# Kernel optimization log

Measured on AMD Instinct MI355X. Metric: run time of the kernel, lower is better.

Reference implementation:

```python
import math
import jax, jax.numpy as jnp
import numpy as np

B, S = 4, 2048
D_MODEL, D_STATE = 1024, 256
KSIZE, CHUNK, STEPS = 5, 16, 2
TOPK, LOOKBACK = 8, 64


def setup_inputs() -> dict:
    key = jax.random.key(0)
    ks = jax.random.split(key, 12)
    gn = lambda k, shape, s: jax.random.normal(k, shape, jnp.float32) * s
    s_in = 1.0 / math.sqrt(D_MODEL)
    s_st = 1.0 / math.sqrt(D_STATE)
    inp = {}
    inp['x'] = gn(ks[0], (B, S, D_MODEL), 1.0)
    inp['Wi'] = gn(ks[1], (D_MODEL, D_STATE), s_in); inp['bi'] = jnp.zeros((D_STATE,), jnp.float32)
    inp['conv_w'] = gn(ks[2], (KSIZE, D_STATE), 1.0 / math.sqrt(KSIZE)); inp['conv_b'] = jnp.zeros((D_STATE,), jnp.float32)
    inp['Wp'] = gn(ks[3], (D_STATE, D_STATE), s_st); inp['bp'] = jnp.zeros((D_STATE,), jnp.float32)
    inp['Wh'] = gn(ks[4], (D_STATE, 3), s_st); inp['bh'] = jnp.zeros((3,), jnp.float32)
    inp['Wq'] = gn(ks[5], (D_STATE, D_STATE), s_st); inp['bq'] = jnp.zeros((D_STATE,), jnp.float32)
    inp['Wk'] = gn(ks[6], (D_STATE, D_STATE), s_st); inp['bk'] = jnp.zeros((D_STATE,), jnp.float32)
    inp['Wv'] = gn(ks[7], (D_STATE, D_STATE), s_st); inp['bv'] = jnp.zeros((D_STATE,), jnp.float32)
    inp['W1'] = gn(ks[8], (4 * D_STATE, D_STATE), 1.0 / math.sqrt(4 * D_STATE)); inp['b1'] = jnp.zeros((D_STATE,), jnp.float32)
    inp['W2'] = gn(ks[9], (D_STATE, D_STATE), s_st); inp['b2'] = jnp.zeros((D_STATE,), jnp.float32)
    # original zero-inits out_proj; use small random so outputs/grads are nontrivial
    inp['Wo'] = gn(ks[10], (D_STATE, D_MODEL), 0.02 * s_st); inp['bo'] = jnp.zeros((D_MODEL,), jnp.float32)
    return inp


def _forward(x, Wi, bi, conv_w, conv_b, Wp, bp, Wh, bh, Wq, bq, Wk, bk, Wv, bv, W1, b1, W2, b2, Wo, bo):
    bsz, seq, _ = x.shape
    dim = Wi.shape[1]
    h = x @ Wi + bi  # [B,S,Dstate]
    # banded window indices: window for token t covers tokens [t-LOOKBACK, t)
    pos = jnp.arange(seq)[:, None] + jnp.arange(LOOKBACK)[None, :]  # index into LOOKBACK-left-padded seq
    valid = (pos - LOOKBACK) >= 0  # [S,L] actual token index = pos - LOOKBACK, always < t
    cidx = jnp.arange(seq)[:, None] + jnp.arange(KSIZE)[None, :]
    scale = 1.0 / math.sqrt(dim)
    for _ in range(STEPS):
        # causal depthwise conv (left pad K-1)
        hp = jnp.pad(h, ((0, 0), (KSIZE - 1, 0), (0, 0)))
        mixed = jnp.einsum('bskd,kd->bsd', hp[:, cidx, :], conv_w) + conv_b
        # phrase pool: chunk means, project, broadcast back to tokens
        ph = h.reshape(bsz, seq // CHUNK, CHUNK, dim).mean(axis=2)
        pb = jnp.repeat(ph @ Wp + bp, CHUNK, axis=1)
        # semantic causal windowed top-k attention
        q = h @ Wq + bq
        k = h @ Wk + bk
        v = h @ Wv + bv
        kp = jnp.pad(k, ((0, 0), (LOOKBACK, 0), (0, 0)))
        scores = jnp.einsum('bsd,bsld->bsl', q, kp[:, pos, :]) * scale  # [B,S,L]
        scores = jnp.where(valid[None], scores, -jnp.inf)
        ts, tr = jax.lax.top_k(scores, TOPK)  # [B,S,K]
        m = ts.max(axis=-1, keepdims=True)
        e = jnp.exp(ts - jnp.where(jnp.isfinite(m), m, 0.0))  # -inf slots -> 0 weight
        w = e / jnp.maximum(e.sum(axis=-1, keepdims=True), 1e-30)  # token 0: all zero
        tok = jnp.clip(jnp.arange(seq)[None, :, None] - LOOKBACK + tr, 0, seq - 1)  # [B,S,K]
        vg = jnp.take_along_axis(v, tok.reshape(bsz, seq * TOPK, 1), axis=1).reshape(bsz, seq, TOPK, dim)
        summ = jnp.einsum('bsk,bskd->bsd', w, vg)
        # update MLP with halt gate
        ui = jnp.concatenate([h, mixed, pb, summ], axis=-1)
        delta = jnp.tanh(ui @ W1 + b1) @ W2 + b2
        gate = jax.nn.sigmoid(h @ Wh + bh)[..., 2:3]  # halt_gate channel
        h = h + delta * gate
    return x + (h @ Wo + bo)


def reference(x, Wi, bi, conv_w, conv_b, Wp, bp, Wh, bh, Wq, bq, Wk, bk, Wv, bv, W1, b1, W2, b2, Wo, bo):
    return _forward(x, Wi, bi, conv_w, conv_b, Wp, bp, Wh, bh, Wq, bq, Wk, bk, Wv, bv, W1, b1, W2, b2, Wo, bo)
```

## Files before the change

### kernel.cpp

```cpp
#include <hip/hip_runtime.h>
#include <math.h>

#define B_    4
#define S_    2048
#define BS_   8192
#define DM_   1024
#define DS_   256
#define LB_   64
#define TOPK_ 8

typedef unsigned short u16;
typedef __bf16 bf16x8 __attribute__((ext_vector_type(8)));
typedef float  f32x4  __attribute__((ext_vector_type(4)));

static __device__ __forceinline__ u16 f2bf(float f) {
    union { float f; unsigned u; } a; a.f = f;
    unsigned u = a.u;
    unsigned r = u + 0x7FFFu + ((u >> 16) & 1u);
    return (u16)(r >> 16);
}
static __device__ __forceinline__ float bf2f(u16 v) {
    union { unsigned u; float f; } a; a.u = ((unsigned)v) << 16; return a.f;
}
static __device__ __forceinline__ unsigned pack2(float a, float b) {
    return (unsigned)f2bf(a) | ((unsigned)f2bf(b) << 16);
}

#define GLD16(g, l) __builtin_amdgcn_global_load_lds(                         \
    (const __attribute__((address_space(1))) void*)(g),                       \
    (__attribute__((address_space(3))) void*)(l), 16, 0, 0)

template<int MF, int EPI>
__device__ __forceinline__ void epilogue(
    f32x4 (&acc)[MF][2], int bm, int bn, int wm, int wn, int lr, int lc,
    const float* __restrict__ bias, void* __restrict__ Cv, int N,
    const void* __restrict__ extra0v, const float* __restrict__ extra1)
{
    #pragma unroll
    for (int i = 0; i < MF; ++i) {
        #pragma unroll
        for (int j = 0; j < 2; ++j) {
            int col = bn + wn * 32 + j * 16 + lr;
            #pragma unroll
            for (int r = 0; r < 4; ++r) {
                int row = bm + wm * (MF * 16) + i * 16 + lc * 4 + r;
                float val = acc[i][j][r] + bias[col];
                if constexpr (EPI == 2) {
                    const u16* e0 = (const u16*)extra0v;
                    val = bf2f(e0[(size_t)row * N + col]) + val * extra1[row];
                    ((u16*)Cv)[(size_t)row * N + col] = f2bf(val);
                } else if constexpr (EPI == 3) {
                    const u16* e0 = (const u16*)extra0v;
                    ((float*)Cv)[(size_t)row * N + col] = bf2f(e0[(size_t)row * N + col]) + val;
                } else {
                    ((u16*)Cv)[(size_t)row * N + col] = f2bf(val);
                }
            }
        }
    }
}

__device__ __forceinline__ void slab_mfma(
    unsigned char* smA, unsigned char* smB, f32x4 (&acc)[2][2],
    int wm, int wn, int lr, int lc)
{
    #pragma unroll
    for (int kg = 0; kg < 8; ++kg) {
        bf16x8 af[2], bfr[2];
        #pragma unroll
        for (int i = 0; i < 2; ++i) {
            int m = wm * 32 + i * 16 + lr;
            af[i] = *reinterpret_cast<const bf16x8*>(
                smA + m * 512 + (((kg * 4 + lc) ^ (m & 15)) * 16));
        }
        #pragma unroll
        for (int j = 0; j < 2; ++j) {
            int n = wn * 32 + j * 16 + lr;
            bfr[j] = *reinterpret_cast<const bf16x8*>(
                smB + n * 512 + (((kg * 4 + lc) ^ (n & 15)) * 16));
        }
        #pragma unroll
        for (int i = 0; i < 2; ++i)
            #pragma unroll
            for (int j = 0; j < 2; ++j)
                acc[i][j] = __builtin_amdgcn_mfma_f32_16x16x32_bf16(
                    af[i], bfr[j], acc[i][j], 0, 0, 0);
    }
}

template<int EPI>
__device__ __forceinline__ void mm256_dev(
    unsigned char* smem, int id, int nb, int gx,
    const u16* __restrict__ A, const u16* __restrict__ Bt,
    const float* __restrict__ bias, void* __restrict__ Cv,
    int N, const void* __restrict__ extra0v, const float* __restrict__ extra1)
{
    unsigned char* smA = smem;
    unsigned char* smB = smem + 32768;

    const int per = nb >> 3;
    const int nid = (id & 7) * per + (id >> 3);
    const int bx  = nid % gx, by = nid / gx;

    const int lane = threadIdx.x & 63, wid = threadIdx.x >> 6;
    const int wm   = wid >> 1, wn = wid & 1;
    const int bm   = by * 64, bn = bx * 64;
    const int lr   = lane & 15, lc = lane >> 4;
    const int lrow2 = lane >> 5;
    const int g_lin = lane & 31;

    #pragma unroll
    for (int t = 0; t < 8; ++t) {
        int rbase = wid * 16 + t * 2;
        int row   = rbase + lrow2;
        int gg    = g_lin ^ (row & 15);
        GLD16(A + (size_t)(bm + row) * 256 + gg * 8, smA + (size_t)rbase * 512);
    }
    #pragma unroll
    for (int t = 0; t < 8; ++t) {
        int rbase = wid * 16 + t * 2;
        int row   = rbase + lrow2;
        int gg    = g_lin ^ (row & 15);
        GLD16(Bt + (size_t)(bn + row) * 256 + gg * 8, smB + (size_t)rbase * 512);
    }
    __syncthreads();

    f32x4 acc[2][2] = {};
    slab_mfma(smA, smB, acc, wm, wn, lr, lc);

    epilogue<2, EPI>(acc, bm, bn, wm, wn, lr, lc, bias, Cv, N, extra0v, extra1);
}

template<int EPI>
__global__ __launch_bounds__(256) void mm256_k(
    const u16* __restrict__ A, const u16* __restrict__ Bt,
    const float* __restrict__ bias, void* __restrict__ Cv,
    int N, int gx,
    const void* __restrict__ extra0v, const float* __restrict__ extra1)
{
    __shared__ __align__(16) unsigned char smem[65536];
    mm256_dev<EPI>(smem, blockIdx.x, gridDim.x, gx, A, Bt, bias, Cv, N,
                   extra0v, extra1);
}

template<int EPI>
__global__ __launch_bounds__(256) void mm1024_k(
    const u16* __restrict__ A, const u16* __restrict__ Bt,
    const float* __restrict__ bias, void* __restrict__ Cv,
    int N, int gx,
    const void* __restrict__ extra0v, const float* __restrict__ extra1)
{
    __shared__ __align__(16) unsigned char smem[65536];
    unsigned char* smA = smem;
    unsigned char* smB = smem + 32768;

    const int nb  = gridDim.x;
    const int per = nb >> 3;
    const int id  = blockIdx.x;
    const int nid = (id & 7) * per + (id >> 3);
    const int bx  = nid % gx, by = nid / gx;

    const int lane = threadIdx.x & 63, wid = threadIdx.x >> 6;
    const int wm   = wid >> 1, wn = wid & 1;
    const int bm   = by * 64, bn = bx * 64;
    const int lr   = lane & 15, lc = lane >> 4;
    const int lrow2 = lane >> 5;
    const int g_lin = lane & 31;

    f32x4 acc[2][2] = {};

    #pragma unroll
    for (int s = 0; s < 4; ++s) {
        if (s) __syncthreads();
        #pragma unroll
        for (int t = 0; t < 8; ++t) {
            int rbase = wid * 16 + t * 2;
            int row   = rbase + lrow2;
            int gg    = g_lin ^ (row & 15);
            GLD16(A + (size_t)(bm + row) * 1024 + s * 256 + gg * 8,
                  smA + (size_t)rbase * 512);
        }
        #pragma unroll
        for (int t = 0; t < 8; ++t) {
            int rbase = wid * 16 + t * 2;
            int row   = rbase + lrow2;
            int gg    = g_lin ^ (row & 15);
            GLD16(Bt + (size_t)(bn + row) * 1024 + s * 256 + gg * 8,
                  smB + (size_t)rbase * 512);
        }
        __syncthreads();
        slab_mfma(smA, smB, acc, wm, wn, lr, lc);
    }

    epilogue<2, EPI>(acc, bm, bn, wm, wn, lr, lc, bias, Cv, N, extra0v, extra1);
}

__global__ __launch_bounds__(256) void mm_ui_k(
    const u16* __restrict__ h, const u16* __restrict__ mixed,
    const u16* __restrict__ php, const u16* __restrict__ summ,
    const u16* __restrict__ W1t, const float* __restrict__ b1,
    u16* __restrict__ t)
{
    __shared__ __align__(16) unsigned char smem[65536];
    unsigned char* smA = smem;
    unsigned char* smB = smem + 32768;

    const int nb  = gridDim.x;
    const int per = nb >> 3;
    const int id  = blockIdx.x;
    const int nid = (id & 7) * per + (id >> 3);
    const int bx  = nid & 3, by = nid >> 2;

    const int lane = threadIdx.x & 63, wid = threadIdx.x >> 6;
    const int wm   = wid >> 1, wn = wid & 1;
    const int bm   = by * 64, bn = bx * 64;
    const int lr   = lane & 15, lc = lane >> 4;
    const int lrow2 = lane >> 5;
    const int g_lin = lane & 31;

    f32x4 acc[2][2] = {};

    #pragma unroll
    for (int s = 0; s < 4; ++s) {
        const u16* Asrc = (s == 0) ? h : (s == 1) ? mixed : (s == 2) ? php : summ;
        if (s) __syncthreads();
        #pragma unroll
        for (int tt = 0; tt < 8; ++tt) {
            int rbase = wid * 16 + tt * 2;
            int row   = rbase + lrow2;
            int gg    = g_lin ^ (row & 15);
            int rs    = bm + row;
            if (s == 2) rs >>= 4;
            GLD16(Asrc + (size_t)rs * 256 + gg * 8, smA + (size_t)rbase * 512);
        }
        #pragma unroll
        for (int tt = 0; tt < 8; ++tt) {
            int rbase = wid * 16 + tt * 2;
            int row   = rbase + lrow2;
            int gg    = g_lin ^ (row & 15);
            GLD16(W1t + (size_t)(bn + row) * 1024 + s * 256 + gg * 8,
                  smB + (size_t)rbase * 512);
        }
        __syncthreads();
        slab_mfma(smA, smB, acc, wm, wn, lr, lc);
    }

    #pragma unroll
    for (int i = 0; i < 2; ++i) {
        #pragma unroll
        for (int j = 0; j < 2; ++j) {
            int col = bn + wn * 32 + j * 16 + lr;
            #pragma unroll
            for (int r = 0; r < 4; ++r) {
                int row = bm + wm * 32 + i * 16 + lc * 4 + r;
                t[(size_t)row * DS_ + col] = f2bf(tanhf(acc[i][j][r] + b1[col]));
            }
        }
    }
}

__device__ __forceinline__ void conv_dev(
    unsigned char* smem, int cid,
    const u16* __restrict__ h, const float* __restrict__ conv_w,
    const float* __restrict__ conv_b, const float* __restrict__ Wh,
    const float* __restrict__ bh, const u16* __restrict__ Wpt,
    const float* __restrict__ bp, u16* __restrict__ mixed,
    u16* __restrict__ php, float* __restrict__ gate)
{
    float* gpart = (float*)smem;
    float* cm    = (float*)(smem + 256);
    const int blk = (cid & 7) * 64 + (cid >> 3);
    const int d = threadIdx.x;
    const int b = blk >> 7;
    const int s0 = (blk & 127) * 16;
    const u16* hb = h + (size_t)b * S_ * DS_;
    u16* mb = mixed + (size_t)b * S_ * DS_;

    const float w0 = conv_w[0 * DS_ + d], w1 = conv_w[1 * DS_ + d],
                w2 = conv_w[2 * DS_ + d], w3 = conv_w[3 * DS_ + d],
                w4 = conv_w[4 * DS_ + d];
    const float cb = conv_b[d];
    const float whd = Wh[d * 3 + 2];

    float a0 = (s0 >= 4) ? bf2f(hb[(size_t)(s0 - 4) * DS_ + d]) : 0.f;
    float a1 = (s0 >= 3) ? bf2f(hb[(size_t)(s0 - 3) * DS_ + d]) : 0.f;
    float a2 = (s0 >= 2) ? bf2f(hb[(size_t)(s0 - 2) * DS_ + d]) : 0.f;
    float a3 = (s0 >= 1) ? bf2f(hb[(size_t)(s0 - 1) * DS_ + d]) : 0.f;

    float sum = 0.f;
    #pragma unroll
    for (int tt = 0; tt < 16; ++tt) {
        int s = s0 + tt;
        float cur = bf2f(hb[(size_t)s * DS_ + d]);
        mb[(size_t)s * DS_ + d] = f2bf(w0 * a0 + w1 * a1 + w2 * a2 + w3 * a3 + w4 * cur + cb);
        sum += cur;
        float g = cur * whd;
        #pragma unroll
        for (int off = 32; off; off >>= 1) g += __shfl_down(g, off);
        if ((d & 63) == 0) gpart[tt * 4 + (d >> 6)] = g;
        a0 = a1; a1 = a2; a2 = a3; a3 = cur;
    }
    cm[d] = sum * (1.f / 16.f);
    __syncthreads();
    if (d < 16) {
        float gg = gpart[d * 4 + 0] + gpart[d * 4 + 1] + gpart[d * 4 + 2] + gpart[d * 4 + 3];
        gate[(size_t)b * S_ + s0 + d] = 1.f / (1.f + expf(-(gg + bh[2])));
    }
    float accp = bp[d];
    const u16* wr = Wpt + (size_t)d * 256;
    #pragma unroll
    for (int k = 0; k < 256; k += 8) {
        bf16x8 w8 = *reinterpret_cast<const bf16x8*>(wr + k);
        accp += cm[k]     * (float)w8[0] + cm[k + 1] * (float)w8[1]
              + cm[k + 2] * (float)w8[2] + cm[k + 3] * (float)w8[3]
              + cm[k + 4] * (float)w8[4] + cm[k + 5] * (float)w8[5]
              + cm[k + 6] * (float)w8[6] + cm[k + 7] * (float)w8[7];
    }
    php[(size_t)blk * DS_ + d] = f2bf(accp);
}

__global__ __launch_bounds__(256) void step_a_k(
    const u16* __restrict__ h, const u16* __restrict__ Wqkvt,
    const float* __restrict__ bqkv, u16* __restrict__ qkv,
    const float* __restrict__ conv_w, const float* __restrict__ conv_b,
    const float* __restrict__ Wh, const float* __restrict__ bh,
    const u16* __restrict__ Wpt, const float* __restrict__ bp,
    u16* __restrict__ mixed, u16* __restrict__ php, float* __restrict__ gate)
{
    __shared__ __align__(16) unsigned char smem[65536];
    if (blockIdx.x < 512) {
        conv_dev(smem, blockIdx.x, h, conv_w, conv_b, Wh, bh,
                 Wpt, bp, mixed, php, gate);
    } else {
        mm256_dev<0>(smem, blockIdx.x - 512, 1536, 12, h, Wqkvt, bqkv, qkv,
                     768, nullptr, nullptr);
    }
}

__global__ __launch_bounds__(256) void scores_k(
    const u16* __restrict__ qkv, float* __restrict__ scores)
{
    __shared__ __align__(16) unsigned char smem[65536];
    unsigned char* smQ = smem;
    unsigned char* smK = smem + 16384;
    float* Sld = reinterpret_cast<float*>(smem);

    const int bid = blockIdx.x;
    const int blk = (bid & 7) * 32 + (bid >> 3);
    const int t0 = blk * 32;
    const int b  = t0 >> 11;
    const int s0 = t0 & (S_ - 1);
    const int tid = threadIdx.x;
    const int lane = tid & 63, wid = tid >> 6;
    const int lr = lane & 15, lc = lane >> 4;
    const int qt  = wid & 1;
    const int ktb = (wid >> 1) * 3;
    const int lrow2 = lane >> 5;
    const int g_lin = lane & 31;

    #pragma unroll
    for (int t = 0; t < 4; ++t) {
        int rbase = wid * 8 + t * 2;
        int row   = rbase + lrow2;
        int gg    = g_lin ^ (row & 15);
        GLD16(qkv + (size_t)(t0 + row) * 768 + gg * 8,
              smQ + (size_t)rbase * 512);
    }
    #pragma unroll
    for (int t = 0; t < 12; ++t) {
        int rbase = wid * 24 + t * 2;
        int row   = rbase + lrow2;
        int krow  = s0 - 64 + row; if (krow < 0) krow = 0;
        int gg    = g_lin ^ (row & 15);
        GLD16(qkv + ((size_t)(b * S_) + krow) * 768 + 256 + gg * 8,
              smK + (size_t)rbase * 512);
    }
    __syncthreads();

    f32x4 acc[3] = {};
    #pragma unroll
    for (int ks = 0; ks < 8; ++ks) {
        int m = qt * 16 + lr;
        bf16x8 af = *reinterpret_cast<const bf16x8*>(
            smQ + m * 512 + (((ks * 4 + lc) ^ (m & 15)) * 16));
        #pragma unroll
        for (int j = 0; j < 3; ++j) {
            int n = (ktb + j) * 16 + lr;
            bf16x8 bv = *reinterpret_cast<const bf16x8*>(
                smK + n * 512 + (((ks * 4 + lc) ^ (n & 15)) * 16));
            acc[j] = __builtin_amdgcn_mfma_f32_16x16x32_bf16(af, bv, acc[j], 0, 0, 0);
        }
    }
    __syncthreads();

    #pragma unroll
    for (int j = 0; j < 3; ++j) {
        int col = (ktb + j) * 16 + lr;
        #pragma unroll
        for (int r = 0; r < 4; ++r) {
            int row = qt * 16 + lc * 4 + r;
            Sld[row * 97 + col] = acc[j][r];
        }
    }
    __syncthreads();

    #pragma unroll
    for (int it = 0; it < 8; ++it) {
        int e = tid + it * 256;
        int i = e >> 6, l = e & 63;
        scores[(size_t)(t0 + i) * 64 + l] = Sld[i * 97 + i + l] * 0.0625f;
    }
}

__global__ __launch_bounds__(256) void select_k(
    const float* __restrict__ scores, const u16* __restrict__ qkv,
    u16* __restrict__ summ)
{
    const int bid = blockIdx.x;
    const int sb  = (bid & 7) * 256 + (bid >> 3);
    const int m   = sb * 4 + (threadIdx.x >> 6);
    const int b = m >> 11;
    const int s = m & (S_ - 1);
    const int lane = threadIdx.x & 63;

    float v = (s - LB_ + lane >= 0) ? scores[(size_t)m * 64 + lane] : -INFINITY;
    int idx = lane;

    #pragma unroll
    for (int k = 2; k <= 64; k <<= 1) {
        #pragma unroll
        for (int j = k >> 1; j > 0; j >>= 1) {
            float ov = __shfl_xor(v, j);
            int   oi = __shfl_xor(idx, j);
            bool mineFirst = (v > ov) || (v == ov && idx < oi);
            bool lowLane  = (lane & j) == 0;
            bool dirFirst = (lane & k) == 0;
            bool keep = (lowLane == dirFirst) ? mineFirst : !mineFirst;
            if (!keep) { v = ov; idx = oi; }
        }
    }

    float vals[TOPK_]; int idxs[TOPK_];
    #pragma unroll
    for (int t = 0; t < TOPK_; ++t) {
        vals[t] = __shfl(v, t);
        idxs[t] = __shfl(idx, t);
    }

    const float mref = (vals[0] == -INFINITY) ? 0.f : vals[0];
    float e[TOPK_], ssum = 0.f;
    #pragma unroll
    for (int t = 0; t < TOPK_; ++t) { e[t] = expf(vals[t] - mref); ssum += e[t]; }
    const float inv = 1.f / fmaxf(ssum, 1e-30f);

    float o0 = 0.f, o1 = 0.f, o2 = 0.f, o3 = 0.f;
    #pragma unroll
    for (int t = 0; t < TOPK_; ++t) {
        float wt = e[t] * inv;
        int tok = s - LB_ + idxs[t];
        tok = min(max(tok, 0), S_ - 1);
        ushort4 vv = *reinterpret_cast<const ushort4*>(
            qkv + ((size_t)(b * S_) + tok) * 768 + 512 + lane * 4);
        o0 += wt * bf2f(vv.x);
        o1 += wt * bf2f(vv.y);
        o2 += wt * bf2f(vv.z);
        o3 += wt * bf2f(vv.w);
    }
    ushort4 pk;
    pk.x = f2bf(o0); pk.y = f2bf(o1); pk.z = f2bf(o2); pk.w = f2bf(o3);
    *reinterpret_cast<ushort4*>(summ + (size_t)m * DS_ + lane * 4) = pk;
}

__global__ __launch_bounds__(256) void prep_all_k(
    const float* __restrict__ x,
    const float* __restrict__ Wi, const float* __restrict__ Wq,
    const float* __restrict__ Wk, const float* __restrict__ Wv,
    const float* __restrict__ Wp, const float* __restrict__ W1,
    const float* __restrict__ W2, const float* __restrict__ Wo,
    const float* __restrict__ bq, const float* __restrict__ bk,
    const float* __restrict__ bv,
    u16* __restrict__ xb,
    u16* __restrict__ Wit, u16* __restrict__ Wqkvt, u16* __restrict__ Wpt,
    u16* __restrict__ W1t, u16* __restrict__ W2t, u16* __restrict__ Wot,
    float* __restrict__ bqkv)
{
    const int bid0 = blockIdx.x;
    if (bid0 < 4096) {
        int i = (bid0 * 256 + threadIdx.x) * 8;
        float4 a = *reinterpret_cast<const float4*>(x + i);
        float4 b = *reinterpret_cast<const float4*>(x + i + 4);
        uint4 g;
        g.x = pack2(a.x, a.y); g.y = pack2(a.z, a.w);
        g.z = pack2(b.x, b.y); g.w = pack2(b.z, b.w);
        *reinterpret_cast<uint4*>(xb + i) = g;
        return;
    }
    const int bid = bid0 - 4096;
    if (bid >= 1088) {
        for (int i = threadIdx.x; i < 768; i += 256) {
            float v = (i < 256) ? bq[i] : (i < 512) ? bk[i - 256] : bv[i - 512];
            bqkv[i] = v;
        }
        return;
    }
    const float* in; u16* out; int K, N, t;
    if (bid < 256)      { in = Wi; out = Wit;             K = 1024; N = 256;  t = bid; }
    else if (bid < 320) { in = Wq; out = Wqkvt;           K = 256;  N = 256;  t = bid - 256; }
    else if (bid < 384) { in = Wk; out = Wqkvt + 256*256; K = 256;  N = 256;  t = bid - 320; }
    else if (bid < 448) { in = Wv; out = Wqkvt + 512*256; K = 256;  N = 256;  t = bid - 384; }
    else if (bid < 512) { in = Wp; out = Wpt;             K = 256;  N = 256;  t = bid - 448; }
    else if (bid < 768) { in = W1; out = W1t;             K = 1024; N = 256;  t = bid - 512; }
    else if (bid < 832) { in = W2; out = W2t;             K = 256;  N = 256;  t = bid - 768; }
    else                { in = Wo; out = Wot;             K = 256;  N = 1024; t = bid - 832; }
    const int tilesX = N >> 5;
    const int n0 = (t % tilesX) * 32, k0 = (t / tilesX) * 32;
    __shared__ float tl[32][33];
    const int cx = threadIdx.x & 31, cy = threadIdx.x >> 5;
    #pragma unroll
    for (int r = 0; r < 32; r += 8)
        tl[cy + r][cx] = in[(size_t)(k0 + cy + r) * N + n0 + cx];
    __syncthreads();
    #pragma unroll
    for (int r = 0; r < 32; r += 8)
        out[(size_t)(n0 + cy + r) * K + k0 + cx] = f2bf(tl[cx][cy + r]);
}

extern "C" void kernel_launch(void* const* d_in, const int* in_sizes, int n_in,
                              void* d_out, int out_size, void* d_ws, size_t ws_size,
                              hipStream_t stream)
{
    const float* x      = (const float*)d_in[0];
    const float* Wi     = (const float*)d_in[1];
    const float* bi     = (const float*)d_in[2];
    const float* conv_w = (const float*)d_in[3];
    const float* conv_b = (const float*)d_in[4];
    const float* Wp     = (const float*)d_in[5];
    const float* bp     = (const float*)d_in[6];
    const float* Wh     = (const float*)d_in[7];
    const float* bh     = (const float*)d_in[8];
    const float* Wq     = (const float*)d_in[9];
    const float* bq     = (const float*)d_in[10];
    const float* Wk     = (const float*)d_in[11];
    const float* bk     = (const float*)d_in[12];
    const float* Wv     = (const float*)d_in[13];
    const float* bv     = (const float*)d_in[14];
    const float* W1     = (const float*)d_in[15];
    const float* b1     = (const float*)d_in[16];
    const float* W2     = (const float*)d_in[17];
    const float* b2     = (const float*)d_in[18];
    const float* Wo     = (const float*)d_in[19];
    const float* bo     = (const float*)d_in[20];
    float* out = (float*)d_out;

    char* p = (char*)d_ws;
    auto alloc = [&](size_t bytes) { char* r = p; p += (bytes + 255) & ~(size_t)255; return r; };

    u16*  xb     = (u16*)alloc((size_t)BS_ * DM_ * 2);
    u16*  h      = (u16*)alloc((size_t)BS_ * DS_ * 2);
    u16*  mixed  = (u16*)alloc((size_t)BS_ * DS_ * 2);
    u16*  qkv    = (u16*)alloc((size_t)BS_ * 768 * 2);
    u16*  sm     = (u16*)alloc((size_t)BS_ * DS_ * 2);
    u16*  tb     = (u16*)alloc((size_t)BS_ * DS_ * 2);
    u16*  php    = (u16*)alloc((size_t)512 * DS_ * 2);
    float* gate  = (float*)alloc((size_t)BS_ * 4);
    float* scores= (float*)alloc((size_t)BS_ * 64 * 4);
    float* bqkv  = (float*)alloc(768 * 4);
    u16* Wit     = (u16*)alloc((size_t)256 * 1024 * 2);
    u16* Wqkvt   = (u16*)alloc((size_t)768 * 256 * 2);
    u16* Wpt     = (u16*)alloc((size_t)256 * 256 * 2);
    u16* W1t     = (u16*)alloc((size_t)256 * 1024 * 2);
    u16* W2t     = (u16*)alloc((size_t)256 * 256 * 2);
    u16* Wot     = (u16*)alloc((size_t)1024 * 256 * 2);

    dim3 blk(256);

    prep_all_k<<<5185, blk, 0, stream>>>(x, Wi, Wq, Wk, Wv, Wp, W1, W2, Wo,
                                         bq, bk, bv, xb,
                                         Wit, Wqkvt, Wpt, W1t, W2t, Wot, bqkv);

    mm1024_k<0><<<512, blk, 0, stream>>>(xb, Wit, bi, h, DS_, 4, nullptr, nullptr);

    for (int step = 0; step < 2; ++step) {
        step_a_k<<<2048, blk, 0, stream>>>(h, Wqkvt, bqkv, qkv,
                                           conv_w, conv_b, Wh, bh, Wpt, bp,
                                           mixed, php, gate);
        scores_k<<<256, blk, 0, stream>>>(qkv, scores);
        select_k<<<2048, blk, 0, stream>>>(scores, qkv, sm);
        mm_ui_k<<<512, blk, 0, stream>>>(h, mixed, php, sm, W1t, b1, tb);
        mm256_k<2><<<512, blk, 0, stream>>>(tb, W2t, b2, h, DS_, 4, h, gate);
    }

    mm256_k<3><<<2048, blk, 0, stream>>>(h, Wot, bo, out, DM_, 16, xb, nullptr);
}
```

Before: 140.9 us.

## Widen GEMM tiles to reuse staged A slabs across multiple B column blocks

Each GEMM block (input projection, QKV, W1, W2, output projection) now covers 128 or 256 output columns instead of 64. It stages the A slab once and restages only the B slab for each extra 64-column sub-tile, and the grids shrink to match. The aim is to cut redundant A loads and the number of blocks launched. The cost is fewer blocks and extra serialized barrier/load phases per block with no overlap of the B restaging. Separately, the scores kernel splits its K-loop across two accumulators to expose more independent MFMA chains.

```diff
diff --git a/kernel.cpp b/kernel.cpp
--- a/kernel.cpp
+++ b/kernel.cpp
@@ -30,20 +30,20 @@
     (const __attribute__((address_space(1))) void*)(g),                       \
     (__attribute__((address_space(3))) void*)(l), 16, 0, 0)
 
-template<int MF, int EPI>
+template<int EPI>
 __device__ __forceinline__ void epilogue(
-    f32x4 (&acc)[MF][2], int bm, int bn, int wm, int wn, int lr, int lc,
+    f32x4 (&acc)[2][2], int bm, int bn, int wm, int wn, int lr, int lc,
     const float* __restrict__ bias, void* __restrict__ Cv, int N,
     const void* __restrict__ extra0v, const float* __restrict__ extra1)
 {
     #pragma unroll
-    for (int i = 0; i < MF; ++i) {
+    for (int i = 0; i < 2; ++i) {
         #pragma unroll
         for (int j = 0; j < 2; ++j) {
             int col = bn + wn * 32 + j * 16 + lr;
             #pragma unroll
             for (int r = 0; r < 4; ++r) {
-                int row = bm + wm * (MF * 16) + i * 16 + lc * 4 + r;
+                int row = bm + wm * 32 + i * 16 + lc * 4 + r;
                 float val = acc[i][j][r] + bias[col];
                 if constexpr (EPI == 2) {
                     const u16* e0 = (const u16*)extra0v;
@@ -60,7 +60,7 @@
     }
 }
 
-__device__ __forceinline__ void slab_mfma(
+__device__ __forceinline__ void slab_mfma1(
     unsigned char* smA, unsigned char* smB, f32x4 (&acc)[2][2],
     int wm, int wn, int lr, int lc)
 {
@@ -88,8 +88,21 @@
     }
 }
 
-template<int EPI>
-__device__ __forceinline__ void mm256_dev(
+__device__ __forceinline__ void stage_slab(
+    unsigned char* sm, const u16* __restrict__ src, int pitch,
+    int wid, int lrow2, int g_lin)
+{
+    #pragma unroll
+    for (int t = 0; t < 8; ++t) {
+        int rbase = wid * 16 + t * 2;
+        int row   = rbase + lrow2;
+        int gg    = g_lin ^ (row & 15);
+        GLD16(src + (size_t)row * pitch + gg * 8, sm + (size_t)rbase * 512);
+    }
+}
+
+template<int H, int EPI>
+__device__ __forceinline__ void mm256r_dev(
     unsigned char* smem, int id, int nb, int gx,
     const u16* __restrict__ A, const u16* __restrict__ Bt,
     const float* __restrict__ bias, void* __restrict__ Cv,
@@ -104,47 +117,44 @@
 
     const int lane = threadIdx.x & 63, wid = threadIdx.x >> 6;
     const int wm   = wid >> 1, wn = wid & 1;
-    const int bm   = by * 64, bn = bx * 64;
+    const int bm   = by * 64, bn = bx * (64 * H);
     const int lr   = lane & 15, lc = lane >> 4;
     const int lrow2 = lane >> 5;
     const int g_lin = lane & 31;
 
-    #pragma unroll
-    for (int t = 0; t < 8; ++t) {
-        int rbase = wid * 16 + t * 2;
-        int row   = rbase + lrow2;
-        int gg    = g_lin ^ (row & 15);
-        GLD16(A + (size_t)(bm + row) * 256 + gg * 8, smA + (size_t)rbase * 512);
-    }
-    #pragma unroll
-    for (int t = 0; t < 8; ++t) {
-        int rbase = wid * 16 + t * 2;
-        int row   = rbase + lrow2;
-        int gg    = g_lin ^ (row & 15);
-        GLD16(Bt + (size_t)(bn + row) * 256 + gg * 8, smB + (size_t)rbase * 512);
-    }
+    stage_slab(smA, A + (size_t)bm * 256, 256, wid, lrow2, g_lin);
+    stage_slab(smB, Bt + (size_t)bn * 256, 256, wid, lrow2, g_lin);
     __syncthreads();
 
-    f32x4 acc[2][2] = {};
-    slab_mfma(smA, smB, acc, wm, wn, lr, lc);
-
-    epilogue<2, EPI>(acc, bm, bn, wm, wn, lr, lc, bias, Cv, N, extra0v, extra1);
-}
-
-template<int EPI>
-__global__ __launch_bounds__(256) void mm256_k(
+    #pragma unroll
+    for (int ht = 0; ht < H; ++ht) {
+        f32x4 acc[2][2] = {};
+        slab_mfma1(smA, smB, acc, wm, wn, lr, lc);
+        if (ht + 1 < H) {
+            __syncthreads();
+            stage_slab(smB, Bt + (size_t)(bn + (ht + 1) * 64) * 256, 256,
+                       wid, lrow2, g_lin);
+        }
+        epilogue<EPI>(acc, bm, bn + ht * 64, wm, wn, lr, lc, bias, Cv, N,
+                      extra0v, extra1);
+        if (ht + 1 < H) __syncthreads();
+    }
+}
+
+template<int H, int EPI>
+__global__ __launch_bounds__(256) void mm256r_k(
     const u16* __restrict__ A, const u16* __restrict__ Bt,
     const float* __restrict__ bias, void* __restrict__ Cv,
     int N, int gx,
     const void* __restrict__ extra0v, const float* __restrict__ extra1)
 {
     __shared__ __align__(16) unsigned char smem[65536];
-    mm256_dev<EPI>(smem, blockIdx.x, gridDim.x, gx, A, Bt, bias, Cv, N,
-                   extra0v, extra1);
+    mm256r_dev<H, EPI>(smem, blockIdx.x, gridDim.x, gx, A, Bt, bias, Cv, N,
+                       extra0v, extra1);
 }
 
 template<int EPI>
-__global__ __launch_bounds__(256) void mm1024_k(
+__global__ __launch_bounds__(256) void mm1024r_k(
     const u16* __restrict__ A, const u16* __restrict__ Bt,
     const float* __restrict__ bias, void* __restrict__ Cv,
     int N, int gx,
@@ -162,37 +172,29 @@
 
     const int lane = threadIdx.x & 63, wid = threadIdx.x >> 6;
     const int wm   = wid >> 1, wn = wid & 1;
-    const int bm   = by * 64, bn = bx * 64;
+    const int bm   = by * 64, bn = bx * 128;
     const int lr   = lane & 15, lc = lane >> 4;
     const int lrow2 = lane >> 5;
     const int g_lin = lane & 31;
 
-    f32x4 acc[2][2] = {};
+    f32x4 acc0[2][2] = {}, acc1[2][2] = {};
 
     #pragma unroll
     for (int s = 0; s < 4; ++s) {
         if (s) __syncthreads();
-        #pragma unroll
-        for (int t = 0; t < 8; ++t) {
-            int rbase = wid * 16 + t * 2;
-            int row   = rbase + lrow2;
-            int gg    = g_lin ^ (row & 15);
-            GLD16(A + (size_t)(bm + row) * 1024 + s * 256 + gg * 8,
-                  smA + (size_t)rbase * 512);
-        }
-        #pragma unroll
-        for (int t = 0; t < 8; ++t) {
-            int rbase = wid * 16 + t * 2;
-            int row   = rbase + lrow2;
-            int gg    = g_lin ^ (row & 15);
-            GLD16(Bt + (size_t)(bn + row) * 1024 + s * 256 + gg * 8,
-                  smB + (size_t)rbase * 512);
-        }
+        stage_slab(smA, A + (size_t)bm * 1024 + s * 256, 1024, wid, lrow2, g_lin);
+        stage_slab(smB, Bt + (size_t)bn * 1024 + s * 256, 1024, wid, lrow2, g_lin);
         __syncthreads();
-        slab_mfma(smA, smB, acc, wm, wn, lr, lc);
-    }
-
-    epilogue<2, EPI>(acc, bm, bn, wm, wn, lr, lc, bias, Cv, N, extra0v, extra1);
+        slab_mfma1(smA, smB, acc0, wm, wn, lr, lc);
+        __syncthreads();
+        stage_slab(smB, Bt + (size_t)(bn + 64) * 1024 + s * 256, 1024,
+                   wid, lrow2, g_lin);
+        __syncthreads();
+        slab_mfma1(smA, smB, acc1, wm, wn, lr, lc);
+    }
+
+    epilogue<EPI>(acc0, bm, bn,      wm, wn, lr, lc, bias, Cv, N, extra0v, extra1);
+    epilogue<EPI>(acc1, bm, bn + 64, wm, wn, lr, lc, bias, Cv, N, extra0v, extra1);
 }
 
 __global__ __launch_bounds__(256) void mm_ui_k(
@@ -209,16 +211,16 @@
     const int per = nb >> 3;
     const int id  = blockIdx.x;
     const int nid = (id & 7) * per + (id >> 3);
-    const int bx  = nid & 3, by = nid >> 2;
+    const int bx  = nid & 1, by = nid >> 1;
 
     const int lane = threadIdx.x & 63, wid = threadIdx.x >> 6;
     const int wm   = wid >> 1, wn = wid & 1;
-    const int bm   = by * 64, bn = bx * 64;
+    const int bm   = by * 64, bn = bx * 128;
     const int lr   = lane & 15, lc = lane >> 4;
     const int lrow2 = lane >> 5;
     const int g_lin = lane & 31;
 
-    f32x4 acc[2][2] = {};
+    f32x4 acc0[2][2] = {}, acc1[2][2] = {};
 
     #pragma unroll
     for (int s = 0; s < 4; ++s) {
@@ -233,27 +235,29 @@
             if (s == 2) rs >>= 4;
             GLD16(Asrc + (size_t)rs * 256 + gg * 8, smA + (size_t)rbase * 512);
         }
-        #pragma unroll
-        for (int tt = 0; tt < 8; ++tt) {
-            int rbase = wid * 16 + tt * 2;
-            int row   = rbase + lrow2;
-            int gg    = g_lin ^ (row & 15);
-            GLD16(W1t + (size_t)(bn + row) * 1024 + s * 256 + gg * 8,
-                  smB + (size_t)rbase * 512);
-        }
+        stage_slab(smB, W1t + (size_t)bn * 1024 + s * 256, 1024, wid, lrow2, g_lin);
         __syncthreads();
-        slab_mfma(smA, smB, acc, wm, wn, lr, lc);
-    }
-
-    #pragma unroll
-    for (int i = 0; i < 2; ++i) {
-        #pragma unroll
-        for (int j = 0; j < 2; ++j) {
-            int col = bn + wn * 32 + j * 16 + lr;
+        slab_mfma1(smA, smB, acc0, wm, wn, lr, lc);
+        __syncthreads();
+        stage_slab(smB, W1t + (size_t)(bn + 64) * 1024 + s * 256, 1024,
+                   wid, lrow2, g_lin);
+        __syncthreads();
+        slab_mfma1(smA, smB, acc1, wm, wn, lr, lc);
+    }
+
+    #pragma unroll
+    for (int half = 0; half < 2; ++half) {
+        f32x4 (&acc)[2][2] = half ? acc1 : acc0;
+        #pragma unroll
+        for (int i = 0; i < 2; ++i) {
             #pragma unroll
-            for (int r = 0; r < 4; ++r) {
-                int row = bm + wm * 32 + i * 16 + lc * 4 + r;
-                t[(size_t)row * DS_ + col] = f2bf(tanhf(acc[i][j][r] + b1[col]));
+            for (int j = 0; j < 2; ++j) {
+                int col = bn + half * 64 + wn * 32 + j * 16 + lr;
+                #pragma unroll
+                for (int r = 0; r < 4; ++r) {
+                    int row = bm + wm * 32 + i * 16 + lc * 4 + r;
+                    t[(size_t)row * DS_ + col] = f2bf(tanhf(acc[i][j][r] + b1[col]));
+                }
             }
         }
     }
@@ -328,12 +332,12 @@
     u16* __restrict__ mixed, u16* __restrict__ php, float* __restrict__ gate)
 {
     __shared__ __align__(16) unsigned char smem[65536];
-    if (blockIdx.x < 512) {
-        conv_dev(smem, blockIdx.x, h, conv_w, conv_b, Wh, bh,
+    if (blockIdx.x < 768) {
+        mm256r_dev<2, 0>(smem, blockIdx.x, 768, 6, h, Wqkvt, bqkv, qkv,
+                         768, nullptr, nullptr);
+    } else {
+        conv_dev(smem, blockIdx.x - 768, h, conv_w, conv_b, Wh, bh,
                  Wpt, bp, mixed, php, gate);
-    } else {
-        mm256_dev<0>(smem, blockIdx.x - 512, 1536, 12, h, Wqkvt, bqkv, qkv,
-                     768, nullptr, nullptr);
     }
 }
 
@@ -377,18 +381,23 @@
     }
     __syncthreads();
 
-    f32x4 acc[3] = {};
-    #pragma unroll
-    for (int ks = 0; ks < 8; ++ks) {
+    f32x4 acc[3] = {}, acc2[3] = {};
+    #pragma unroll
+    for (int ks = 0; ks < 8; ks += 2) {
         int m = qt * 16 + lr;
-        bf16x8 af = *reinterpret_cast<const bf16x8*>(
-            smQ + m * 512 + (((ks * 4 + lc) ^ (m & 15)) * 16));
+        bf16x8 af0 = *reinterpret_cast<const bf16x8*>(
+            smQ + m * 512 + ((((ks + 0) * 4 + lc) ^ (m & 15)) * 16));
+        bf16x8 af1 = *reinterpret_cast<const bf16x8*>(
+            smQ + m * 512 + ((((ks + 1) * 4 + lc) ^ (m & 15)) * 16));
         #pragma unroll
         for (int j = 0; j < 3; ++j) {
             int n = (ktb + j) * 16 + lr;
-            bf16x8 bv = *reinterpret_cast<const bf16x8*>(
-                smK + n * 512 + (((ks * 4 + lc) ^ (n & 15)) * 16));
-            acc[j] = __builtin_amdgcn_mfma_f32_16x16x32_bf16(af, bv, acc[j], 0, 0, 0);
+            bf16x8 bv0 = *reinterpret_cast<const bf16x8*>(
+                smK + n * 512 + ((((ks + 0) * 4 + lc) ^ (n & 15)) * 16));
+            bf16x8 bv1 = *reinterpret_cast<const bf16x8*>(
+                smK + n * 512 + ((((ks + 1) * 4 + lc) ^ (n & 15)) * 16));
+            acc[j]  = __builtin_amdgcn_mfma_f32_16x16x32_bf16(af0, bv0, acc[j], 0, 0, 0);
+            acc2[j] = __builtin_amdgcn_mfma_f32_16x16x32_bf16(af1, bv1, acc2[j], 0, 0, 0);
         }
     }
     __syncthreads();
@@ -399,7 +408,7 @@
         #pragma unroll
         for (int r = 0; r < 4; ++r) {
             int row = qt * 16 + lc * 4 + r;
-            Sld[row * 97 + col] = acc[j][r];
+            Sld[row * 97 + col] = acc[j][r] + acc2[j][r];
         }
     }
     __syncthreads();
@@ -578,17 +587,17 @@
                                          bq, bk, bv, xb,
                                          Wit, Wqkvt, Wpt, W1t, W2t, Wot, bqkv);
 
-    mm1024_k<0><<<512, blk, 0, stream>>>(xb, Wit, bi, h, DS_, 4, nullptr, nullptr);
+    mm1024r_k<0><<<256, blk, 0, stream>>>(xb, Wit, bi, h, DS_, 2, nullptr, nullptr);
 
     for (int step = 0; step < 2; ++step) {
-        step_a_k<<<2048, blk, 0, stream>>>(h, Wqkvt, bqkv, qkv,
+        step_a_k<<<1280, blk, 0, stream>>>(h, Wqkvt, bqkv, qkv,
                                            conv_w, conv_b, Wh, bh, Wpt, bp,
                                            mixed, php, gate);
         scores_k<<<256, blk, 0, stream>>>(qkv, scores);
         select_k<<<2048, blk, 0, stream>>>(scores, qkv, sm);
-        mm_ui_k<<<512, blk, 0, stream>>>(h, mixed, php, sm, W1t, b1, tb);
-        mm256_k<2><<<512, blk, 0, stream>>>(tb, W2t, b2, h, DS_, 4, h, gate);
-    }
-
-    mm256_k<3><<<2048, blk, 0, stream>>>(h, Wot, bo, out, DM_, 16, xb, nullptr);
-}
+        mm_ui_k<<<256, blk, 0, stream>>>(h, mixed, php, sm, W1t, b1, tb);
+        mm256r_k<2, 2><<<256, blk, 0, stream>>>(tb, W2t, b2, h, DS_, 2, h, gate);
+    }
+
+    mm256r_k<4, 3><<<512, blk, 0, stream>>>(h, Wot, bo, out, DM_, 4, xb, nullptr);
+}
```

After: 148.6 us, median of 2. 5.5% more time.
